# Optimization experiments

Hardware: AMD Instinct MI355X
Metric: run time of the kernel (lower is better)

The kernel has to match this reference:

```python
import jax, jax.numpy as jnp
import numpy as np

B, P, O, C = 32, 65536, 32, 2
THRESH = 0.35
VAR = (0.1, 0.2)
LOC_W, LANDM_W = 2.0, 1.0
ALPHA, GAMMA = 0.25, 1.5
EPS = 1e-7


def setup_inputs():
    key = jax.random.key(0)
    k = jax.random.split(key, 8)
    loc_data = jax.random.normal(k[0], (B, P, 4), jnp.float32) * 0.1
    conf_data = jax.random.normal(k[1], (B, P, C), jnp.float32)
    landm_data = jax.random.normal(k[2], (B, P, 10), jnp.float32) * 0.1
    # priors in center form (cx, cy, w, h)
    cxcy = jax.random.uniform(k[3], (P, 2), minval=0.05, maxval=0.95)
    wh = jax.random.uniform(k[4], (P, 2), minval=0.02, maxval=0.3)
    priors = jnp.concatenate([cxcy, wh], axis=-1).astype(jnp.float32)
    # targets [B, O, 15]: corner box (4) + 5 landmarks (10) + label (1, in {-1, +1})
    xy1 = jax.random.uniform(k[5], (B, O, 2), minval=0.0, maxval=0.7)
    bwh = jax.random.uniform(k[6], (B, O, 2), minval=0.05, maxval=0.25)
    boxes = jnp.concatenate([xy1, xy1 + bwh], axis=-1)
    landms = jnp.tile(xy1 + bwh * 0.5, (1, 1, 5))
    labels = (jax.random.randint(k[7], (B, O, 1), 0, 2) * 2 - 1).astype(jnp.float32)
    targets = jnp.concatenate([boxes, landms, labels], axis=-1)
    return {"loc_data": loc_data, "conf_data": conf_data, "landm_data": landm_data,
            "priors": priors, "targets": targets}


def point_form(pr):  # (cx,cy,w,h) -> (x1,y1,x2,y2)
    return jnp.concatenate([pr[:, :2] - pr[:, 2:] / 2, pr[:, :2] + pr[:, 2:] / 2], -1)


def pairwise_iou(a, b):  # a [O,4], b [P,4] corner form -> [O,P]
    lt = jnp.maximum(a[:, None, :2], b[None, :, :2])
    rb = jnp.minimum(a[:, None, 2:], b[None, :, 2:])
    whd = jnp.clip(rb - lt, 0.0)
    inter = whd[..., 0] * whd[..., 1]
    area_a = ((a[:, 2] - a[:, 0]) * (a[:, 3] - a[:, 1]))[:, None]
    area_b = ((b[:, 2] - b[:, 0]) * (b[:, 3] - b[:, 1]))[None, :]
    return inter / (area_a + area_b - inter)


def encode_landm(matched, priors):  # matched [P,10], priors [P,4] center form
    m = matched.reshape(P, 5, 2)
    g = (m - priors[:, None, :2]) / (VAR[0] * priors[:, None, 2:])
    return g.reshape(P, 10)


def match_one(truths, landms, labels, priors_pf, priors):
    ov = pairwise_iou(truths, priors_pf)                       # [O,P]
    best_prior_idx = jnp.argmax(ov, axis=1)                    # [O] best prior per gt
    best_truth_overlap = ov.max(axis=0)                        # [P]
    best_truth_idx = jnp.argmax(ov, axis=0)                    # [P]
    # ensure every gt keeps its best prior
    best_truth_overlap = best_truth_overlap.at[best_prior_idx].set(2.0)
    best_truth_idx = best_truth_idx.at[best_prior_idx].set(jnp.arange(truths.shape[0]))
    loc_t = truths[best_truth_idx]                             # [P,4] matched gt boxes (corner)
    conf = jnp.where(best_truth_overlap < THRESH, 0.0, labels[best_truth_idx])
    landm_t = encode_landm(landms[best_truth_idx], priors)     # [P,10]
    return loc_t, conf, landm_t


def decode(loc, priors):  # SSD center-form decode -> corner boxes
    xy = priors[..., :2] + loc[..., :2] * VAR[0] * priors[..., 2:]
    wh = priors[..., 2:] * jnp.exp(loc[..., 2:] * VAR[1])
    return jnp.concatenate([xy - wh / 2, xy + wh / 2], -1)


def giou(b1, b2):  # elementwise GIoU, corner form
    area1 = (b1[..., 2] - b1[..., 0]) * (b1[..., 3] - b1[..., 1])
    area2 = (b2[..., 2] - b2[..., 0]) * (b2[..., 3] - b2[..., 1])
    iw = jnp.clip(jnp.minimum(b1[..., 2], b2[..., 2]) - jnp.maximum(b1[..., 0], b2[..., 0]), 0.0)
    ih = jnp.clip(jnp.minimum(b1[..., 3], b2[..., 3]) - jnp.maximum(b1[..., 1], b2[..., 1]), 0.0)
    inter = iw * ih
    union = area1 + area2 - inter
    iou = inter / (union + EPS)
    ew = jnp.maximum(b1[..., 2], b2[..., 2]) - jnp.minimum(b1[..., 0], b2[..., 0])
    eh = jnp.maximum(b1[..., 3], b2[..., 3]) - jnp.minimum(b1[..., 1], b2[..., 1])
    enc = ew * eh
    return iou - (enc - union) / (enc + EPS)


def smooth_l1(x):
    ax = jnp.abs(x)
    return jnp.where(ax < 1.0, 0.5 * x * x, ax - 0.5)


def reference(loc_data, conf_data, landm_data, priors, targets):
    # matching uses detached (.data) priors/targets in the original
    priors_c = jax.lax.stop_gradient(priors)
    targets_c = jax.lax.stop_gradient(targets)
    truths, landms, labels = targets_c[..., :4], targets_c[..., 4:14], targets_c[..., 14]
    priors_pf = point_form(priors_c)
    loc_t, conf_raw, landm_t = jax.vmap(match_one, in_axes=(0, 0, 0, None, None))(
        truths, landms, labels, priors_pf, priors_c)  # [B,P,4],[B,P],[B,P,10]

    # landmark loss on pos1 = conf > 0 (label +1: face with landmarks)
    pos1 = conf_raw > 0
    N1 = jnp.maximum(pos1.sum().astype(jnp.float32), 1.0)
    loss_landm = (smooth_l1(landm_data - landm_t).sum(-1) * pos1).sum() * LANDM_W

    # loc GIoU loss on pos = conf != 0
    pos = conf_raw != 0
    conf_t = pos.astype(jnp.int32)  # conf_t[pos] = 1, background 0
    dec = decode(loc_data, priors_c[None])  # [B,P,4]
    loss_l = jnp.where(pos, 1.0 - giou(dec, loc_t), 0.0).sum() * LOC_W

    # focal loss over all B*P anchors (size_average=False -> sum)
    logp = jax.nn.log_softmax(conf_data, axis=-1)
    logp_t = jnp.take_along_axis(logp, conf_t[..., None], axis=-1)[..., 0]
    p_t = jnp.exp(logp_t)
    loss_c = (-ALPHA * (1.0 - p_t) ** GAMMA * logp_t).sum()

    # original normalizes loss_l and loss_c by num_pos_landm sum (N), landm by N1 (==N)
    N = N1
    return (loss_l / N, loss_c / N, loss_landm / N1)
```

## Files before the change

kernel.cpp:

```cpp
#include <hip/hip_runtime.h>
#include <cstdint>

#define B_ 32
#define P_ 65536
#define O_ 32
#define GX_ 64
#define KC_ 4
#define THRESH_ 0.35f
#define VAR0 0.1f
#define VAR1 0.2f
#define EPS_ 1e-7f
#define ALPHA_ 0.25f

struct WSHdr {
  unsigned long long gkey[B_ * O_];
  float4 part[GX_ * B_];
};

__device__ __forceinline__ float frcp(float x) { return __builtin_amdgcn_rcpf(x); }

template <int CTRL>
__device__ __forceinline__ unsigned long long dpp_max_u64(unsigned long long k) {
  int lo = __builtin_amdgcn_update_dpp((int)(unsigned)k, (int)(unsigned)k,
                                       CTRL, 0xF, 0xF, false);
  int hi = __builtin_amdgcn_update_dpp((int)(k >> 32), (int)(k >> 32),
                                       CTRL, 0xF, 0xF, false);
  unsigned long long o = ((unsigned long long)(unsigned)hi << 32) | (unsigned)lo;
  return o > k ? o : k;
}

__global__ void init_ws(WSHdr* ws) {
  int t = blockIdx.x * blockDim.x + threadIdx.x;
  if (t < B_ * O_) ws->gkey[t] = 0ull;
}

template <bool BIG>
__global__ __launch_bounds__(256, 8) void k_match(const float* __restrict__ priors,
                                                  const float* __restrict__ targets,
                                                  WSHdr* __restrict__ ws,
                                                  uint2* __restrict__ pb) {
  __shared__ float tsh[O_][5];
  __shared__ unsigned long long kq[O_][17];
  const int b = blockIdx.y;
  const int tid = threadIdx.x;
  const int lane = tid & 63, wid = tid >> 6;
  if (tid < O_) {
    const float* trow = targets + ((size_t)b * O_ + tid) * 15;
    float x1 = trow[0], y1 = trow[1], x2 = trow[2], y2 = trow[3];
    tsh[tid][0] = x1; tsh[tid][1] = y1; tsh[tid][2] = x2; tsh[tid][3] = y2;
    tsh[tid][4] = (x2 - x1) * (y2 - y1);
  }
  __syncthreads();

  float px1[KC_], py1[KC_], px2[KC_], py2[KC_], pa[KC_], bov[KC_];
  int bidx[KC_];
  unsigned pinv[KC_];
  #pragma unroll
  for (int k = 0; k < KC_; ++k) {
    unsigned p = (unsigned)((blockIdx.x + k * GX_) * 256 + tid);
    pinv[k] = 0xFFFFFFFFu - p;
    float4 pr = reinterpret_cast<const float4*>(priors)[p];
    px1[k] = pr.x - pr.z * 0.5f; py1[k] = pr.y - pr.w * 0.5f;
    px2[k] = pr.x + pr.z * 0.5f; py2[k] = pr.y + pr.w * 0.5f;
    pa[k] = (px2[k] - px1[k]) * (py2[k] - py1[k]);
    bov[k] = -1.f; bidx[k] = 0;
  }

  #pragma unroll 4
  for (int o = 0; o < O_; ++o) {
    const float x1 = tsh[o][0], y1 = tsh[o][1], x2 = tsh[o][2], y2 = tsh[o][3];
    const float ta = tsh[o][4];
    float tiou = 0.f;
    unsigned tinv = pinv[0];
    #pragma unroll
    for (int k = 0; k < KC_; ++k) {
      float iw = fmaxf(fminf(x2, px2[k]) - fmaxf(x1, px1[k]), 0.f);
      float ih = fmaxf(fminf(y2, py2[k]) - fmaxf(y1, py1[k]), 0.f);
      float inter = iw * ih;
      float iou = inter * frcp(ta + pa[k] - inter);
      if (iou > bov[k]) { bov[k] = iou; bidx[k] = o; }
      if (iou > tiou)   { tiou = iou; tinv = pinv[k]; }
    }
    unsigned long long key = ((unsigned long long)__float_as_uint(tiou) << 32) |
                             (unsigned long long)tinv;
    key = dpp_max_u64<0x128>(key);
    key = dpp_max_u64<0x124>(key);
    key = dpp_max_u64<0x122>(key);
    key = dpp_max_u64<0x121>(key);
    if ((lane & 15) == 0) kq[o][wid * 4 + (lane >> 4)] = key;
  }

  if (BIG) {
    #pragma unroll
    for (int k = 0; k < KC_; ++k)
      pb[(size_t)b * P_ + (0xFFFFFFFFu - pinv[k])] =
          make_uint2(__float_as_uint(bov[k]), (unsigned)bidx[k]);
  }
  __syncthreads();
  if (tid < O_) {
    unsigned long long best = kq[tid][0];
    #pragma unroll
    for (int s = 1; s < 16; ++s) {
      unsigned long long v = kq[tid][s];
      if (v > best) best = v;
    }
    atomicMax(&ws->gkey[(size_t)b * O_ + tid], best);
  }
}

template <bool BIG>
__global__ __launch_bounds__(256) void k_loss(const float* __restrict__ loc_data,
                                              const float* __restrict__ conf_data,
                                              const float* __restrict__ landm_data,
                                              const float* __restrict__ priors,
                                              const float* __restrict__ targets,
                                              WSHdr* __restrict__ ws,
                                              const uint2* __restrict__ pb) {
  __shared__ float tx1[O_], ty1[O_], tx2[O_], ty2[O_], tarea[O_], tlbl[O_];
  __shared__ float tlm[O_][10];
  __shared__ unsigned int fprior[O_];
  __shared__ float4 wsum[4];
  const int b = blockIdx.y;
  const int tid = threadIdx.x;
  if (tid < O_) {
    const float* trow = targets + ((size_t)b * O_ + tid) * 15;
    float x1 = trow[0], y1 = trow[1], x2 = trow[2], y2 = trow[3];
    tx1[tid] = x1; ty1[tid] = y1; tx2[tid] = x2; ty2[tid] = y2;
    tarea[tid] = (x2 - x1) * (y2 - y1);
    #pragma unroll
    for (int k = 0; k < 10; ++k) tlm[tid][k] = trow[4 + k];
    tlbl[tid] = trow[14];
    fprior[tid] = 0xFFFFFFFFu - (unsigned)(ws->gkey[(size_t)b * O_ + tid] & 0xFFFFFFFFull);
  }
  __syncthreads();

  float vx = 0.f, vy = 0.f, vz = 0.f, vw = 0.f;

  #pragma unroll
  for (int k = 0; k < KC_; ++k) {
    const int p = (blockIdx.x + k * GX_) * 256 + tid;
    const size_t bp = (size_t)b * P_ + p;
    float4 pr = reinterpret_cast<const float4*>(priors)[p];

    float ov;
    int idx;
    if (BIG) {
      uint2 v = pb[bp];
      ov = __uint_as_float(v.x);
      idx = (int)v.y;
    } else {
      float px1 = pr.x - pr.z * 0.5f, py1 = pr.y - pr.w * 0.5f;
      float px2 = pr.x + pr.z * 0.5f, py2 = pr.y + pr.w * 0.5f;
      float parea = (px2 - px1) * (py2 - py1);
      float bov = -1.f;
      int bidx = 0;
      #pragma unroll 8
      for (int o = 0; o < O_; ++o) {
        float iw = fmaxf(fminf(tx2[o], px2) - fmaxf(tx1[o], px1), 0.f);
        float ih = fmaxf(fminf(ty2[o], py2) - fmaxf(ty1[o], py1), 0.f);
        float inter = iw * ih;
        float iou = inter * frcp(tarea[o] + parea - inter);
        if (iou > bov) { bov = iou; bidx = o; }
      }
      ov = bov; idx = bidx;
    }
    int fi = -1;
    #pragma unroll
    for (int j = 0; j < O_; ++j)
      if (fprior[j] == (unsigned)p) fi = j;
    if (fi >= 0) { idx = fi; ov = 2.0f; }

    const bool pos = !(ov < THRESH_);
    const bool pos1 = pos && (tlbl[idx] > 0.f);

    float2 cf = reinterpret_cast<const float2*>(conf_data)[bp];
    float mx = fmaxf(cf.x, cf.y);
    float lse = mx + __logf(1.f + __expf(-fabsf(cf.x - cf.y)));
    float logpt = (pos ? cf.y : cf.x) - lse;
    float pt = __expf(logpt);
    float om = 1.f - pt;
    vy += -ALPHA_ * om * sqrtf(om) * logpt;

    if (pos) {
      float4 loc = reinterpret_cast<const float4*>(loc_data)[bp];
      float dx = pr.x + loc.x * VAR0 * pr.z;
      float dy = pr.y + loc.y * VAR0 * pr.w;
      float dw = pr.z * __expf(loc.z * VAR1);
      float dh = pr.w * __expf(loc.w * VAR1);
      float b1x1 = dx - dw * 0.5f, b1y1 = dy - dh * 0.5f;
      float b1x2 = dx + dw * 0.5f, b1y2 = dy + dh * 0.5f;
      float b2x1 = tx1[idx], b2y1 = ty1[idx], b2x2 = tx2[idx], b2y2 = ty2[idx];
      float a1 = (b1x2 - b1x1) * (b1y2 - b1y1);
      float a2 = (b2x2 - b2x1) * (b2y2 - b2y1);
      float iw = fmaxf(fminf(b1x2, b2x2) - fmaxf(b1x1, b2x1), 0.f);
      float ih = fmaxf(fminf(b1y2, b2y2) - fmaxf(b1y1, b2y1), 0.f);
      float inter = iw * ih;
      float uni = a1 + a2 - inter;
      float iou = inter * frcp(uni + EPS_);
      float ew = fmaxf(b1x2, b2x2) - fminf(b1x1, b2x1);
      float eh = fmaxf(b1y2, b2y2) - fminf(b1y1, b2y1);
      float enc = ew * eh;
      float g = iou - (enc - uni) * frcp(enc + EPS_);
      vx += 1.f - g;
    }
    if (pos1) {
      vw += 1.f;
      const float* lmrow = landm_data + bp * 10;
      float rw = frcp(VAR0 * pr.z);
      float rh = frcp(VAR0 * pr.w);
      float llm = 0.f;
      #pragma unroll
      for (int q = 0; q < 5; ++q) {
        float2 d = *reinterpret_cast<const float2*>(lmrow + q * 2);
        float ex = d.x - (tlm[idx][2 * q] - pr.x) * rw;
        float ey = d.y - (tlm[idx][2 * q + 1] - pr.y) * rh;
        float ax = fabsf(ex), ay = fabsf(ey);
        llm += (ax < 1.f) ? 0.5f * ex * ex : ax - 0.5f;
        llm += (ay < 1.f) ? 0.5f * ey * ey : ay - 0.5f;
      }
      vz += llm;
    }
  }

  #pragma unroll
  for (int i = 32; i > 0; i >>= 1) {
    vx += __shfl_xor(vx, i);
    vy += __shfl_xor(vy, i);
    vz += __shfl_xor(vz, i);
    vw += __shfl_xor(vw, i);
  }
  const int wave = tid >> 6, lane = tid & 63;
  if (lane == 0) wsum[wave] = make_float4(vx, vy, vz, vw);
  __syncthreads();
  if (tid == 0) {
    float sx = 0.f, sy = 0.f, sz = 0.f, sw = 0.f;
    #pragma unroll
    for (int w = 0; w < 4; ++w) {
      sx += wsum[w].x; sy += wsum[w].y; sz += wsum[w].z; sw += wsum[w].w;
    }
    ws->part[(size_t)blockIdx.y * GX_ + blockIdx.x] = make_float4(sx, sy, sz, sw);
  }
}

__global__ __launch_bounds__(256) void k_final(const WSHdr* __restrict__ ws,
                                               float* __restrict__ out) {
  __shared__ double sh[4][4];
  const int tid = threadIdx.x;
  double sx = 0.0, sy = 0.0, sz = 0.0, sw = 0.0;
  for (int i = tid; i < GX_ * B_; i += 256) {
    float4 v = ws->part[i];
    sx += v.x; sy += v.y; sz += v.z; sw += v.w;
  }
  #pragma unroll
  for (int i = 32; i > 0; i >>= 1) {
    sx += __shfl_xor(sx, i);
    sy += __shfl_xor(sy, i);
    sz += __shfl_xor(sz, i);
    sw += __shfl_xor(sw, i);
  }
  const int wave = tid >> 6, lane = tid & 63;
  if (lane == 0) { sh[wave][0] = sx; sh[wave][1] = sy; sh[wave][2] = sz; sh[wave][3] = sw; }
  __syncthreads();
  if (tid == 0) {
    double ax = 0, ay = 0, az = 0, aw = 0;
    #pragma unroll
    for (int w = 0; w < 4; ++w) { ax += sh[w][0]; ay += sh[w][1]; az += sh[w][2]; aw += sh[w][3]; }
    double n1 = aw < 1.0 ? 1.0 : aw;
    out[0] = (float)(2.0 * ax / n1);
    out[1] = (float)(ay / n1);
    out[2] = (float)(az / n1);
  }
}

extern "C" void kernel_launch(void* const* d_in, const int* in_sizes, int n_in,
                              void* d_out, int out_size, void* d_ws, size_t ws_size,
                              hipStream_t stream) {
  (void)in_sizes; (void)n_in; (void)out_size;
  const float* loc     = (const float*)d_in[0];
  const float* conf    = (const float*)d_in[1];
  const float* landm   = (const float*)d_in[2];
  const float* priors  = (const float*)d_in[3];
  const float* targets = (const float*)d_in[4];
  WSHdr* ws = (WSHdr*)d_ws;
  uint2* pb = (uint2*)((char*)d_ws + sizeof(WSHdr));
  float* out = (float*)d_out;
  const bool big = ws_size >= sizeof(WSHdr) + (size_t)B_ * P_ * sizeof(uint2);

  hipLaunchKernelGGL(init_ws, dim3(4), dim3(256), 0, stream, ws);
  dim3 grid(GX_, B_);
  if (big) {
    hipLaunchKernelGGL(k_match<true>, grid, dim3(256), 0, stream, priors, targets, ws, pb);
    hipLaunchKernelGGL(k_loss<true>, grid, dim3(256), 0, stream,
                       loc, conf, landm, priors, targets, ws, pb);
  } else {
    hipLaunchKernelGGL(k_match<false>, grid, dim3(256), 0, stream, priors, targets, ws, pb);
    hipLaunchKernelGGL(k_loss<false>, grid, dim3(256), 0, stream,
                       loc, conf, landm, priors, targets, ws, pb);
  }
  hipLaunchKernelGGL(k_final, dim3(1), dim3(256), 0, stream, ws, out);
}
```

Measured before the change: 79.87 us.

## Split 64-bit DPP argmax into float and index passes; map forced priors via LDS table

The per-gt wave reduction in k_match previously ran a 64-bit packed key max through DPP, which costs two DPP moves plus a 64-bit compare per step. It now does a float max pass, then a 32-bit index max pass restricted to lanes holding the max. In k_loss, each thread no longer scans 32 forced-prior slots per prior. A single thread builds a per-block byte map from prior to gt index, and every thread does one LDS lookup. The launch-bounds occupancy hint on k_match is also dropped. The serial single-thread map build adds a barrier and some latency, and tie handling among equal IoUs in the reduction may differ slightly.

New measurement: 77.00 us. 1.04x faster.

```diff
diff --git a/kernel.cpp b/kernel.cpp
--- a/kernel.cpp
+++ b/kernel.cpp
@@ -20,13 +20,14 @@
 __device__ __forceinline__ float frcp(float x) { return __builtin_amdgcn_rcpf(x); }
 
 template <int CTRL>
-__device__ __forceinline__ unsigned long long dpp_max_u64(unsigned long long k) {
-  int lo = __builtin_amdgcn_update_dpp((int)(unsigned)k, (int)(unsigned)k,
-                                       CTRL, 0xF, 0xF, false);
-  int hi = __builtin_amdgcn_update_dpp((int)(k >> 32), (int)(k >> 32),
-                                       CTRL, 0xF, 0xF, false);
-  unsigned long long o = ((unsigned long long)(unsigned)hi << 32) | (unsigned)lo;
-  return o > k ? o : k;
+__device__ __forceinline__ float dpp_fmax(float v) {
+  int s = __builtin_amdgcn_update_dpp(0, __float_as_int(v), CTRL, 0xF, 0xF, true);
+  return fmaxf(v, __int_as_float(s));
+}
+template <int CTRL>
+__device__ __forceinline__ unsigned dpp_umax(unsigned v) {
+  unsigned u = (unsigned)__builtin_amdgcn_update_dpp(0, (int)v, CTRL, 0xF, 0xF, true);
+  return u > v ? u : v;
 }
 
 __global__ void init_ws(WSHdr* ws) {
@@ -35,10 +36,10 @@
 }
 
 template <bool BIG>
-__global__ __launch_bounds__(256, 8) void k_match(const float* __restrict__ priors,
-                                                  const float* __restrict__ targets,
-                                                  WSHdr* __restrict__ ws,
-                                                  uint2* __restrict__ pb) {
+__global__ __launch_bounds__(256) void k_match(const float* __restrict__ priors,
+                                               const float* __restrict__ targets,
+                                               WSHdr* __restrict__ ws,
+                                               uint2* __restrict__ pb) {
   __shared__ float tsh[O_][5];
   __shared__ unsigned long long kq[O_][17];
   const int b = blockIdx.y;
@@ -81,13 +82,19 @@
       if (iou > bov[k]) { bov[k] = iou; bidx[k] = o; }
       if (iou > tiou)   { tiou = iou; tinv = pinv[k]; }
     }
-    unsigned long long key = ((unsigned long long)__float_as_uint(tiou) << 32) |
-                             (unsigned long long)tinv;
-    key = dpp_max_u64<0x128>(key);
-    key = dpp_max_u64<0x124>(key);
-    key = dpp_max_u64<0x122>(key);
-    key = dpp_max_u64<0x121>(key);
-    if ((lane & 15) == 0) kq[o][wid * 4 + (lane >> 4)] = key;
+    float m = tiou;
+    m = dpp_fmax<0x128>(m);
+    m = dpp_fmax<0x124>(m);
+    m = dpp_fmax<0x122>(m);
+    m = dpp_fmax<0x121>(m);
+    unsigned cand = (tiou == m) ? tinv : 0u;
+    cand = dpp_umax<0x128>(cand);
+    cand = dpp_umax<0x124>(cand);
+    cand = dpp_umax<0x122>(cand);
+    cand = dpp_umax<0x121>(cand);
+    if ((lane & 15) == 0)
+      kq[o][wid * 4 + (lane >> 4)] =
+          ((unsigned long long)__float_as_uint(m) << 32) | (unsigned long long)cand;
   }
 
   if (BIG) {
@@ -118,10 +125,13 @@
                                               const uint2* __restrict__ pb) {
   __shared__ float tx1[O_], ty1[O_], tx2[O_], ty2[O_], tarea[O_], tlbl[O_];
   __shared__ float tlm[O_][10];
-  __shared__ unsigned int fprior[O_];
+  __shared__ unsigned fp_s[O_];
+  __shared__ unsigned char fmap[KC_ * 256];
   __shared__ float4 wsum[4];
   const int b = blockIdx.y;
   const int tid = threadIdx.x;
+  #pragma unroll
+  for (int k = 0; k < KC_; ++k) fmap[k * 256 + tid] = 0xFF;
   if (tid < O_) {
     const float* trow = targets + ((size_t)b * O_ + tid) * 15;
     float x1 = trow[0], y1 = trow[1], x2 = trow[2], y2 = trow[3];
@@ -130,7 +140,16 @@
     #pragma unroll
     for (int k = 0; k < 10; ++k) tlm[tid][k] = trow[4 + k];
     tlbl[tid] = trow[14];
-    fprior[tid] = 0xFFFFFFFFu - (unsigned)(ws->gkey[(size_t)b * O_ + tid] & 0xFFFFFFFFull);
+    fp_s[tid] = 0xFFFFFFFFu - (unsigned)(ws->gkey[(size_t)b * O_ + tid] & 0xFFFFFFFFull);
+  }
+  __syncthreads();
+  if (tid == 0) {
+    for (int j = 0; j < O_; ++j) {
+      unsigned fp = fp_s[j];
+      unsigned c = fp >> 8;
+      if ((c & (GX_ - 1)) == (unsigned)blockIdx.x)
+        fmap[(c >> 6) * 256 + (fp & 255)] = (unsigned char)j;
+    }
   }
   __syncthreads();
 
@@ -164,11 +183,8 @@
       }
       ov = bov; idx = bidx;
     }
-    int fi = -1;
-    #pragma unroll
-    for (int j = 0; j < O_; ++j)
-      if (fprior[j] == (unsigned)p) fi = j;
-    if (fi >= 0) { idx = fi; ov = 2.0f; }
+    unsigned char fj = fmap[k * 256 + tid];
+    if (fj != 0xFF) { idx = (int)fj; ov = 2.0f; }
 
     const bool pos = !(ov < THRESH_);
     const bool pos1 = pos && (tlbl[idx] > 0.f);
```
